# Kernel tuning notes

Measured on AMD Instinct MI355X. Metric: run time of the kernel, lower is better.

The kernel has to match this reference:

```python
import jax, jax.numpy as jnp
import numpy as np

jax.config.update("jax_enable_x64", True)

# Module constants (from MySDELayer.call / run_model)
NUM_TRAJ = 512
DT = 2.0 ** (-8)          # deltat
NSTEPS = 255              # len(arange(0,1,DT)) - 1
OMEGA = 5.0265            # params[0]
GAMMA = 0.36              # params[2]
SQG = float(np.sqrt(GAMMA))


def setup_inputs() -> dict:
    key = jax.random.key(0)
    k1, k2 = jax.random.split(key)
    inputs = jax.random.normal(k1, (32, 1), dtype=jnp.float32)
    # unit-normal Wiener increments; scaled by sqrt(DT) inside reference
    wvec = jax.random.normal(k2, (32 * NUM_TRAJ, NSTEPS, 2), dtype=jnp.float32)
    return {"inputs": inputs, "wvec": wvec}


def _sde_probs(eps, dw):
    """Euler-Maruyama integration of the Genois qubit heterodyne SDE in Bloch
    coordinates (d=3 state, m=2 Wiener channels, complex128 as in the original),
    followed by unwrap to rho and Pauli-expectation probabilities.
    eps: [N] complex128 (per-trajectory middle parameter, e.g. detuning)
    dw:  [N, NSTEPS, 2] complex128 Wiener increments (stddev sqrt(DT))
    returns probs [N, NSTEPS+1, 6] float64
    """
    N = eps.shape[0]
    x0 = jnp.broadcast_to(jnp.array([0.0, 0.0, 1.0], dtype=jnp.complex128), (N, 3))

    def step(x, dwt):  # x: [N,3], dwt: [N,2]
        xx, yy, zz = x[:, 0], x[:, 1], x[:, 2]
        # drift: Rabi drive OMEGA about x, detuning eps about z, dephasing GAMMA
        drift = jnp.stack([
            -eps * yy - GAMMA * xx,
            eps * xx - OMEGA * zz - GAMMA * yy,
            OMEGA * yy,
        ], axis=1)
        # heterodyne measurement backaction (two quadratures)
        b1 = SQG * jnp.stack([-xx * zz, -yy * zz, 1.0 - zz * zz], axis=1)
        b2 = SQG * jnp.stack([-yy, xx, jnp.zeros_like(xx)], axis=1)
        xn = x + drift * DT + b1 * dwt[:, 0:1] + b2 * dwt[:, 1:2]
        return xn, xn

    _, xs = jax.lax.scan(step, x0, jnp.swapaxes(dw, 0, 1))  # [NSTEPS, N, 3]
    xvec = jnp.concatenate([x0[None], xs], axis=0)           # [T, N, 3]
    xvec = jnp.transpose(xvec, (1, 0, 2))                    # [N, T, 3]

    # unwrap_x_to_rho: rho = 0.5*(I + r.sigma) as length-4 vec
    rho = jnp.stack([
        0.5 * (1.0 + xvec[..., 2]),
        0.5 * (xvec[..., 0] - 1j * xvec[..., 1]),
        0.5 * (xvec[..., 0] + 1j * xvec[..., 1]),
        0.5 * (1.0 - xvec[..., 2]),
    ], axis=-1)                                              # [N, T, 4]

    # calc_exp with Pauli matrices
    ex = jnp.real(rho[..., 1] + rho[..., 2])
    ey = jnp.real(1j * (rho[..., 1] - rho[..., 2]))
    ez = jnp.real(rho[..., 0] - rho[..., 3])
    px, py, pz = 0.5 * (ex + 1.0), 0.5 * (ey + 1.0), 0.5 * (ez + 1.0)
    return jnp.stack([px, 1.0 - px, py, 1.0 - py, pz, 1.0 - pz], axis=2)  # [N,T,6]


def reference(inputs, wvec):
    B = inputs.shape[0]
    # tf.tile(inputs, [num_traj, 1])[:, 0] -> trajectory-major replication
    eps = jnp.tile(inputs, (NUM_TRAJ, 1))[:, 0].astype(jnp.complex128)  # [N]
    dw = (wvec * np.sqrt(DT)).astype(jnp.complex128)                    # [N,255,2]
    probs = _sde_probs(eps, dw)                                         # [N,T,6]
    probs_by_params = probs.reshape(B, NUM_TRAJ, probs.shape[1], 6)
    return jnp.mean(probs_by_params, axis=1)                            # [B,T,6]
```

## Files before the change

### kernel.cpp

```cpp
#include <hip/hip_runtime.h>

#define NSTEPS 255
#define TPTS   256
#define NTRAJ  16384
#define NBLK   256
#define CH     15

#define GAMMA_F 0.36f
#define OMEGA_F 5.0265f
#define DT_F    0.00390625f
#define CW      0.0375f
#define GD      (GAMMA_F * DT_F)
#define OD      (OMEGA_F * DT_F)

#define PITCH  520

typedef __fp16 half2v __attribute__((ext_vector_type(2)));
typedef float  f32x2  __attribute__((ext_vector_type(2)));

__device__ __forceinline__ unsigned pk2(float a, float b) {
  half2v h = __builtin_amdgcn_cvt_pkrtz(a, b);
  return __builtin_bit_cast(unsigned, h);
}

#define STEP2(w2, ii_) {                                                        \
  const float w0  = (w2).x * CW;                                                \
  const f32x2 w1n = nCW2 * (w2).y;                        \
  const f32x2 sw  = __builtin_shufflevector(v, v, 1, 0);             \
  f32x2 t = __builtin_elementwise_fma(epack, sw, v);                            \
  t = __builtin_elementwise_fma(mGD2, v, t);                                    \
  const f32x2 p   = v * z;                                                      \
  const f32x2 mw0 = {-w0, -w0};                                                 \
  t = __builtin_elementwise_fma(p, mw0, t);                                     \
  t = __builtin_elementwise_fma(sw, w1n, t);                                    \
  t[1] = __builtin_fmaf(-OD, z, t[1]);                                          \
  const float a_ = __builtin_fmaf(OD, v[1], z);                                 \
  const float r_ = __builtin_fmaf(-(z * z), w0, w0);                            \
  v = t; z = a_ + r_;                                                           \
  *(uint2*)(sb + (ii_) * PITCH) = make_uint2(pk2(v[0], v[1]), pk2(z, 0.0f));    \
}

#define LOADC(BUF, CHUNK_) {                                                    \
  _Pragma("unroll")                                                             \
  for (int i_ = 0; i_ < CH; ++i_) BUF[i_] = wrow[(CHUNK_) * CH + i_];           \
}

#define PROC(BUF) {                                                             \
  _Pragma("unroll")                                                             \
  for (int i_ = 0; i_ < CH; ++i_) STEP2(BUF[i_], i_)                            \
  sb += CH * PITCH;                                                             \
}

__global__ __launch_bounds__(64) void sde_integrate(const float* __restrict__ inp,
                                                    const float* __restrict__ wvec,
                                                    float* __restrict__ partial) {
  __shared__ alignas(16) char smem[NSTEPS * PITCH];
  const int g = blockIdx.x, l = threadIdx.x;
  const float eps = inp[l & 31];
  const f32x2 epack = {-eps * DT_F, eps * DT_F};
  const f32x2 mGD2  = {-GD, -GD};
  const f32x2 nCW2  = {-CW, CW};

  const float2* __restrict__ wrow =
      reinterpret_cast<const float2*>(wvec) + (size_t)(g * 64 + l) * NSTEPS;
  char* sb = smem + l * 8;

  f32x2 v = {0.0f, 0.0f};
  float z = 1.0f;

  float2 bufA[CH], bufB[CH], bufC[CH];

  LOADC(bufA, 0);
  LOADC(bufB, 1);
  #pragma unroll 1
  for (int k = 0; k < 5; ++k) {
    LOADC(bufC, 3 * k + 2); PROC(bufA);
    LOADC(bufA, 3 * k + 3); PROC(bufB);
    LOADC(bufB, 3 * k + 4); PROC(bufC);
  }
  PROC(bufA);
  PROC(bufB);

  __syncthreads();

  #pragma unroll
  for (int k = 0; k < 4; ++k) {
    const int s = l + 64 * k;
    if (s < NSTEPS) {
      const char* rb = smem + (size_t)s * PITCH;
      float fx = 0.0f, fy = 0.0f, fz = 0.0f;
      #pragma unroll
      for (int j = 0; j < 64; ++j) {
        const uint2 u = *(const uint2*)(rb + j * 8);
        const half2v xy = __builtin_bit_cast(half2v, u.x);
        const half2v zp = __builtin_bit_cast(half2v, u.y);
        fx += (float)xy[0];
        fy += (float)xy[1];
        fz += (float)zp[0];
      }
      float* p = partial + ((size_t)g * NSTEPS + s) * 3;
      p[0] = fx; p[1] = fy; p[2] = fz;
    }
  }
}

__global__ __launch_bounds__(256) void sde_finalize(const float* __restrict__ partial,
                                                    float* __restrict__ out) {
  const int idx = blockIdx.x * blockDim.x + threadIdx.x;
  const int b = idx >> 8;
  const int t = idx & 255;
  float* o = out + (size_t)idx * 6;

  if (t == 0) {
    o[0] = 0.5f; o[1] = 0.5f; o[2] = 0.5f; o[3] = 0.5f;
    o[4] = 1.0f; o[5] = 0.0f;
    return;
  }

  float sx = 0.0f, sy = 0.0f, sz = 0.0f;
  #pragma unroll
  for (int j = 0; j < 8; ++j) {
    const float* p = partial + ((size_t)(b * 8 + j) * NSTEPS + (t - 1)) * 3;
    sx += p[0]; sy += p[1]; sz += p[2];
  }
  const float inv = 1.0f / 512.0f;
  const float mx = sx * inv, my = sy * inv, mz = sz * inv;
  o[0] = 0.5f * (1.0f + mx);
  o[1] = 0.5f * (1.0f - mx);
  o[2] = 0.5f * (1.0f + my);
  o[3] = 0.5f * (1.0f - my);
  o[4] = 0.5f * (1.0f + mz);
  o[5] = 0.5f * (1.0f - mz);
}

extern "C" void kernel_launch(void* const* d_in, const int* in_sizes, int n_in,
                              void* d_out, int out_size, void* d_ws, size_t ws_size,
                              hipStream_t stream) {
  (void)in_sizes; (void)n_in; (void)out_size; (void)ws_size;
  const float* inp  = (const float*)d_in[0];
  const float* wvec = (const float*)d_in[1];
  float* out     = (float*)d_out;
  float* partial = (float*)d_ws;

  sde_integrate<<<NBLK, 64, 0, stream>>>(inp, wvec, partial);
  sde_finalize<<<32, 256, 0, stream>>>(partial, out);
}
```

Baseline: 23.01 us.

## Coalesce Wiener increment loads via double-buffered LDS transpose tiles

Each thread used to stream its own trajectory row of Wiener increments straight from global memory, so every load instruction touched many scattered rows. Now 16 lanes cooperatively read contiguous 128-byte segments of each row and stage them into double-buffered LDS tiles. Each thread then reads back its own 16 steps as float4 values. This trades more LDS traffic and a larger shared footprint, which only fits in a large LDS, for coalesced global reads. It relies on the block being a single wavefront, since there is no barrier between the tile writes and reads.

```diff
diff --git a/kernel.cpp b/kernel.cpp
--- a/kernel.cpp
+++ b/kernel.cpp
@@ -4,7 +4,7 @@
 #define TPTS   256
 #define NTRAJ  16384
 #define NBLK   256
-#define CH     15
+#define ROWB   2040
 
 #define GAMMA_F 0.36f
 #define OMEGA_F 5.0265f
@@ -14,6 +14,10 @@
 #define OD      (OMEGA_F * DT_F)
 
 #define PITCH  520
+#define STATEB 132608
+
+#define WROW  144
+#define WTILE (64 * WROW)
 
 typedef __fp16 half2v __attribute__((ext_vector_type(2)));
 typedef float  f32x2  __attribute__((ext_vector_type(2)));
@@ -23,9 +27,9 @@
   return __builtin_bit_cast(unsigned, h);
 }
 
-#define STEP2(w2, ii_) {                                                        \
-  const float w0  = (w2).x * CW;                                                \
-  const f32x2 w1n = nCW2 * (w2).y;                        \
+#define STEP2(wx_, wy_, ii_) {                                                  \
+  const float w0  = (wx_) * CW;                                                 \
+  const f32x2 w1n = nCW2 * (wy_);                         \
   const f32x2 sw  = __builtin_shufflevector(v, v, 1, 0);             \
   f32x2 t = __builtin_elementwise_fma(epack, sw, v);                            \
   t = __builtin_elementwise_fma(mGD2, v, t);                                    \
@@ -40,46 +44,72 @@
   *(uint2*)(sb + (ii_) * PITCH) = make_uint2(pk2(v[0], v[1]), pk2(z, 0.0f));    \
 }
 
-#define LOADC(BUF, CHUNK_) {                                                    \
+#define GLOAD(co) {                                                             \
   _Pragma("unroll")                                                             \
-  for (int i_ = 0; i_ < CH; ++i_) BUF[i_] = wrow[(CHUNK_) * CH + i_];           \
+  for (int i_ = 0; i_ < 16; ++i_)                                               \
+    r2[i_] = *(const float2*)(wbp + (size_t)i_ * (4 * ROWB) + (co));            \
+}
+#define GLOADP(co) {                                                            \
+  if ((l & 15) != 15) {                                                         \
+    _Pragma("unroll")                                                           \
+    for (int i_ = 0; i_ < 16; ++i_)                                             \
+      r2[i_] = *(const float2*)(wbp + (size_t)i_ * (4 * ROWB) + (co));          \
+  }                                                                             \
 }
 
-#define PROC(BUF) {                                                             \
+#define LDSW(WB) {                                                              \
   _Pragma("unroll")                                                             \
-  for (int i_ = 0; i_ < CH; ++i_) STEP2(BUF[i_], i_)                            \
-  sb += CH * PITCH;                                                             \
+  for (int i_ = 0; i_ < 16; ++i_)                                               \
+    *(float2*)((WB) + wl + i_ * (4 * WROW)) = r2[i_];                           \
+}
+
+#define CHUNKN(WB, NK) {                                                        \
+  _Pragma("unroll")                                                             \
+  for (int p_ = 0; p_ < 8; ++p_) {                                              \
+    const float4 wv = *(const float4*)((WB) + rl + p_ * 16);                    \
+    STEP2(wv.x, wv.y, 2 * p_);                                                  \
+    if (2 * p_ + 1 < (NK)) STEP2(wv.z, wv.w, 2 * p_ + 1);                       \
+  }                                                                             \
+  sb += (NK) * PITCH;                                                           \
 }
 
 __global__ __launch_bounds__(64) void sde_integrate(const float* __restrict__ inp,
                                                     const float* __restrict__ wvec,
                                                     float* __restrict__ partial) {
-  __shared__ alignas(16) char smem[NSTEPS * PITCH];
+  __shared__ alignas(16) char smem[STATEB + 2 * WTILE];
   const int g = blockIdx.x, l = threadIdx.x;
   const float eps = inp[l & 31];
   const f32x2 epack = {-eps * DT_F, eps * DT_F};
   const f32x2 mGD2  = {-GD, -GD};
   const f32x2 nCW2  = {-CW, CW};
 
-  const float2* __restrict__ wrow =
-      reinterpret_cast<const float2*>(wvec) + (size_t)(g * 64 + l) * NSTEPS;
+  const char* wbp = (const char*)wvec
+      + (size_t)(g * 64 + (l >> 4)) * ROWB + (l & 15) * 8;
+  char* const wt0 = smem + STATEB;
+  char* const wt1 = wt0 + WTILE;
+  const unsigned wl = (unsigned)((l >> 4) * WROW + (l & 15) * 8);
+  const unsigned rl = (unsigned)(l * WROW);
   char* sb = smem + l * 8;
 
   f32x2 v = {0.0f, 0.0f};
   float z = 1.0f;
+  float2 r2[16];
 
-  float2 bufA[CH], bufB[CH], bufC[CH];
+  GLOAD(0);
+  LDSW(wt0);
+  GLOAD(128);
+  CHUNKN(wt0, 16);
 
-  LOADC(bufA, 0);
-  LOADC(bufB, 1);
   #pragma unroll 1
-  for (int k = 0; k < 5; ++k) {
-    LOADC(bufC, 3 * k + 2); PROC(bufA);
-    LOADC(bufA, 3 * k + 3); PROC(bufB);
-    LOADC(bufB, 3 * k + 4); PROC(bufC);
+  for (int c = 1; c <= 14; ++c) {
+    char* const wb = (c & 1) ? wt1 : wt0;
+    LDSW(wb);
+    if (c < 14) { GLOAD(128 * (c + 1)); }
+    else        { GLOADP(1920); }
+    CHUNKN(wb, 16);
   }
-  PROC(bufA);
-  PROC(bufB);
+  LDSW(wt1);
+  CHUNKN(wt1, 15);
 
   __syncthreads();
 
```

After: 29.49 us. 1.28x slower.
